# Kernel tuning notes

Hardware: AMD Instinct MI355X
Metric: run time of the kernel (lower is better)

## Reference

```python
import jax, jax.numpy as jnp
import numpy as np

NEG_SLOPE = 0.2
EPS = 1e-16


def gat_conv(x, edge_index, W, att_src, att_dst, bias, heads, out_ch, concat):
    """PyG-style GATConv (eval mode, add_self_loops=True)."""
    N = x.shape[0]
    h = (x @ W).reshape(N, heads, out_ch)              # [N,H,C]
    loop = jnp.arange(N, dtype=edge_index.dtype)
    src = jnp.concatenate([edge_index[0], loop])       # [E+N]
    dst = jnp.concatenate([edge_index[1], loop])
    a_src = jnp.sum(h * att_src, axis=-1)              # [N,H]
    a_dst = jnp.sum(h * att_dst, axis=-1)
    e = jax.nn.leaky_relu(a_src[src] + a_dst[dst], NEG_SLOPE)  # [E+N,H]
    # segment softmax over destination nodes
    m = jax.ops.segment_max(e, dst, num_segments=N)
    e = jnp.exp(e - m[dst])
    s = jax.ops.segment_sum(e, dst, num_segments=N)
    alpha = e / (s[dst] + EPS)                         # [E+N,H]
    msg = h[src] * alpha[..., None]                    # [E+N,H,C]
    out = jax.ops.segment_sum(msg, dst, num_segments=N)  # [N,H,C]
    out = out.reshape(N, heads * out_ch) if concat else out.mean(axis=1)
    return out + bias


def setup_inputs() -> dict:
    key = jax.random.key(0)
    ks = jax.random.split(key, 11)
    N, F, E = 100000, 128, 1600000
    H1, C1 = 4, 16
    H2, C2 = 1, 16
    return {
        "x": jax.random.normal(ks[0], (N, F), dtype=jnp.float32),
        "edge_index": jax.random.randint(ks[1], (2, E), 0, N, dtype=jnp.int64) if jax.config.jax_enable_x64 else jax.random.randint(ks[1], (2, E), 0, N).astype(jnp.int32),
        "W1": jax.random.normal(ks[2], (F, H1 * C1), dtype=jnp.float32) * 0.1,
        "att_src1": jax.random.normal(ks[3], (H1, C1), dtype=jnp.float32) * 0.1,
        "att_dst1": jax.random.normal(ks[4], (H1, C1), dtype=jnp.float32) * 0.1,
        "bias1": jax.random.normal(ks[5], (H1 * C1,), dtype=jnp.float32) * 0.1,
        "W2": jax.random.normal(ks[6], (H1 * C1, H2 * C2), dtype=jnp.float32) * 0.1,
        "att_src2": jax.random.normal(ks[7], (H2, C2), dtype=jnp.float32) * 0.1,
        "att_dst2": jax.random.normal(ks[8], (H2, C2), dtype=jnp.float32) * 0.1,
        "bias2": jax.random.normal(ks[9], (C2,), dtype=jnp.float32) * 0.1,
    }


def reference(x, edge_index, W1, att_src1, att_dst1, bias1, W2, att_src2, att_dst2, bias2):
    # dropout is identity in eval mode
    h = gat_conv(x, edge_index, W1, att_src1, att_dst1, bias1, heads=4, out_ch=16, concat=True)
    h = jax.nn.elu(h)
    h = gat_conv(h, edge_index, W2, att_src2, att_dst2, bias2, heads=1, out_ch=16, concat=False)
    return jax.nn.log_softmax(h, axis=1)
```

## Files before the change

### kernel.cpp

```cpp
#include <hip/hip_runtime.h>
#include <hip/hip_fp16.h>
#include <hip/hip_bf16.h>
#include <math.h>


#define LRELU(v) ((v) > 0.f ? (v) : 0.2f * (v))
#define BSH 8
#define BCAP 5120
#define CHK 2048
#define CAP1 64
#define CAP2 64

typedef __attribute__((ext_vector_type(8))) short short8;
typedef __attribute__((ext_vector_type(4))) float float4v;

static __device__ __forceinline__ short f2bf(float f) {
    __hip_bfloat16 b = __float2bfloat16(f);
    return *reinterpret_cast<short*>(&b);
}

__global__ __launch_bounds__(256) void k_scatter(const int* __restrict__ ei, int* __restrict__ cursor,
                                                 int* __restrict__ stage, int E, int NBK) {
    __shared__ int sval[CHK];
    __shared__ int gaddr[CHK];
    __shared__ int hist[512];
    __shared__ int lbase[512];
    __shared__ int cnt2[512];
    __shared__ int gdelta[512];
    __shared__ int sA[512];
    int tid = threadIdx.x;
    int e0 = blockIdx.x * CHK;
    int nedge = E - e0; if (nedge > CHK) nedge = CHK;

    for (int i = tid; i < 512; i += 256) { hist[i] = 0; cnt2[i] = 0; }
    __syncthreads();
    for (int j = tid; j < nedge; j += 256) {
        int d = ei[E + e0 + j];
        atomicAdd(&hist[d >> BSH], 1);
    }
    __syncthreads();
    sA[tid] = hist[tid]; sA[tid + 256] = hist[tid + 256];
    __syncthreads();
    for (int off = 1; off < 512; off <<= 1) {
        int r0 = sA[tid] + ((tid >= off) ? sA[tid - off] : 0);
        int r1 = sA[tid + 256] + ((tid + 256 >= off) ? sA[tid + 256 - off] : 0);
        __syncthreads();
        sA[tid] = r0; sA[tid + 256] = r1;
        __syncthreads();
    }
    for (int i = tid; i < 512; i += 256) lbase[i] = sA[i] - hist[i];
    __syncthreads();
    for (int b = tid; b < NBK; b += 256) {
        int c = hist[b];
        if (c > 0) {
            int rel = atomicAdd(&cursor[b], c);
            gdelta[b] = b * BCAP + rel - lbase[b];
        }
    }
    __syncthreads();
    for (int j = tid; j < nedge; j += 256) {
        int s = ei[e0 + j];
        int d = ei[E + e0 + j];
        int b = d >> BSH;
        int r = atomicAdd(&cnt2[b], 1);
        int slot = lbase[b] + r;
        sval[slot]  = s | ((d & ((1 << BSH) - 1)) << 17);
        gaddr[slot] = gdelta[b] + slot;
    }
    __syncthreads();
    for (int s = tid; s < nedge; s += 256) stage[gaddr[s]] = sval[s];
}

__global__ __launch_bounds__(256) void k_build(const int* __restrict__ stage,
                                               const int* __restrict__ cursor,
                                               int* __restrict__ row_start,
                                               int* __restrict__ csr,
                                               const float* __restrict__ W1,
                                               const float* __restrict__ att_src,
                                               const float* __restrict__ att_dst,
                                               float* __restrict__ Wc,
                                               int NBK, int E, int N) {
    __shared__ int cnt[256];
    __shared__ int lb[256];
    __shared__ int cur[256];
    __shared__ int sA[256];
    int b = blockIdx.x, tid = threadIdx.x;
    int nodes0 = b << BSH;
    int nnodes = N - nodes0; if (nnodes > 256) nnodes = 256;
    int partial = 0;
    for (int i = tid; i < b; i += 256) partial += cursor[i];
    sA[tid] = partial;
    __syncthreads();
    for (int off = 128; off >= 1; off >>= 1) {
        if (tid < off) sA[tid] += sA[tid + off];
        __syncthreads();
    }
    int ebase = sA[0];
    int ecnt = cursor[b];
    __syncthreads();
    if (b == 0) {
        if (tid == 0) row_start[N] = E + N;
        for (int i = tid; i < 16 * 128; i += 256) {
            int col = i >> 7, k = i & 127;
            float v = 0.f;
            if (col < 8) {
                int h = col & 3;
                const float* att = (col < 4) ? att_src : att_dst;
                #pragma unroll
                for (int c = 0; c < 16; c++) v += W1[k * 64 + h * 16 + c] * att[h * 16 + c];
            }
            Wc[i] = v;
        }
    }
    const int* sbk = stage + b * BCAP;
    cnt[tid] = (tid < nnodes) ? 1 : 0;
    __syncthreads();
    for (int e = tid; e < ecnt; e += 256) {
        int l = (sbk[e] >> 17) & 255;
        atomicAdd(&cnt[l], 1);
    }
    __syncthreads();
    int myc = cnt[tid];
    sA[tid] = myc;
    __syncthreads();
    for (int off = 1; off < 256; off <<= 1) {
        int r = sA[tid] + ((tid >= off) ? sA[tid - off] : 0);
        __syncthreads();
        sA[tid] = r;
        __syncthreads();
    }
    int gb = ebase + nodes0;
    lb[tid] = sA[tid] - myc;
    cur[tid] = 1;
    __syncthreads();
    if (tid < nnodes) {
        row_start[nodes0 + tid] = gb + lb[tid];
        csr[gb + lb[tid]] = nodes0 + tid;
    }
    __syncthreads();
    for (int e = tid; e < ecnt; e += 256) {
        int v = sbk[e];
        int l = (v >> 17) & 255;
        int src = v & 0x1FFFF;
        int r = atomicAdd(&cur[l], 1);
        csr[gb + lb[l] + r] = src;
    }
}

__global__ __launch_bounds__(256) void k_gemm1(const float* __restrict__ x,
                                               const float* __restrict__ W1,
                                               const float* __restrict__ Wc,
                                               __half* __restrict__ h1, float* __restrict__ a_src,
                                               float* __restrict__ a_dst, int N) {
    __shared__ short wt[80 * 136];
    int tid = threadIdx.x;
    for (int i = tid; i < 128 * 64; i += 256) {
        int k = i >> 6, c = i & 63;
        wt[c * 136 + k] = f2bf(W1[i]);
    }
    for (int i = tid; i < 16 * 128; i += 256) {
        int col = i >> 7, k = i & 127;
        wt[(64 + col) * 136 + k] = f2bf(Wc[i]);
    }
    __syncthreads();
    int wave = tid >> 6, lane = tid & 63;
    int m = lane & 15, q = lane >> 4;
    int nbase = blockIdx.x * 64 + wave * 16;
    int anode = nbase + m;
    bool rowok = anode < N;
    const float* xrow = x + (size_t)(rowok ? anode : 0) * 128 + q * 8;

    float4v acc[5];
    #pragma unroll
    for (int ct = 0; ct < 5; ct++)
        #pragma unroll
        for (int r = 0; r < 4; r++) acc[ct][r] = 0.f;

    #pragma unroll
    for (int kc = 0; kc < 4; kc++) {
        float4 u0 = make_float4(0.f, 0.f, 0.f, 0.f), u1 = u0;
        if (rowok) {
            u0 = *(const float4*)(xrow + kc * 32);
            u1 = *(const float4*)(xrow + kc * 32 + 4);
        }
        short8 af;
        af[0] = f2bf(u0.x); af[1] = f2bf(u0.y); af[2] = f2bf(u0.z); af[3] = f2bf(u0.w);
        af[4] = f2bf(u1.x); af[5] = f2bf(u1.y); af[6] = f2bf(u1.z); af[7] = f2bf(u1.w);
        #pragma unroll
        for (int ct = 0; ct < 5; ct++) {
            short8 bf = *(const short8*)&wt[(ct * 16 + m) * 136 + kc * 32 + q * 8];
            acc[ct] = __builtin_amdgcn_mfma_f32_16x16x32_bf16(af, bf, acc[ct], 0, 0, 0);
        }
    }
    #pragma unroll
    for (int ct = 0; ct < 4; ct++) {
        #pragma unroll
        for (int r = 0; r < 4; r++) {
            int n = nbase + q * 4 + r;
            if (n < N) h1[(size_t)n * 64 + ct * 16 + m] = __float2half(acc[ct][r]);
        }
    }
    #pragma unroll
    for (int r = 0; r < 4; r++) {
        int n = nbase + q * 4 + r;
        if (n < N) {
            float v = acc[4][r];
            if (m < 4) a_src[n * 4 + m] = v;
            else if (m < 8) a_dst[n * 4 + (m - 4)] = v;
        }
    }
}

__global__ __launch_bounds__(256) void k_agg1(const int* __restrict__ row_start,
                                              const int* __restrict__ csr_src,
                                              const float* __restrict__ a_src,
                                              const float* __restrict__ a_dst,
                                              const __half* __restrict__ h1,
                                              const float* __restrict__ bias,
                                              float* __restrict__ out1, int N) {
    __shared__ int   sidx[16][CAP1];
    __shared__ float sval[16][CAP1 * 4];
    int tid = threadIdx.x;
    int wave = tid >> 6, lane = tid & 63;
    int quad = lane >> 4, l16 = lane & 15;
    int slot = wave * 4 + quad;
    int node = blockIdx.x * 16 + slot;
    if (node >= N) return;
    int row = row_start[node];
    int deg = row_start[node + 1] - row;
    float4 ad = ((const float4*)a_dst)[node];
    float s0 = 0.f, s1 = 0.f, s2 = 0.f, s3 = 0.f;
    for (int j = l16; j < deg; j += 16) {
        int s = csr_src[row + j];
        float4 as = ((const float4*)a_src)[s];
        float e0 = __expf(LRELU(as.x + ad.x));
        float e1 = __expf(LRELU(as.y + ad.y));
        float e2 = __expf(LRELU(as.z + ad.z));
        float e3 = __expf(LRELU(as.w + ad.w));
        if (j < CAP1) {
            sidx[slot][j] = s;
            *(float4*)&sval[slot][j * 4] = make_float4(e0, e1, e2, e3);
        }
        s0 += e0; s1 += e1; s2 += e2; s3 += e3;
    }
    #pragma unroll
    for (int m = 1; m < 16; m <<= 1) {
        s0 += __shfl_xor(s0, m, 64);
        s1 += __shfl_xor(s1, m, 64);
        s2 += __shfl_xor(s2, m, 64);
        s3 += __shfl_xor(s3, m, 64);
    }
    int myh = l16 >> 2;
    float ssv = myh == 0 ? s0 : myh == 1 ? s1 : myh == 2 ? s2 : s3;
    float adm = myh == 0 ? ad.x : myh == 1 ? ad.y : myh == 2 ? ad.z : ad.w;
    float iv = 1.f / (ssv + 1e-16f);
    float A0 = 0.f, A1 = 0.f, A2 = 0.f, A3 = 0.f;
    float B0 = 0.f, B1 = 0.f, B2 = 0.f, B3 = 0.f;
    int dc = deg < CAP1 ? deg : CAP1;
    int j = 0;
    for (; j + 8 <= dc; j += 8) {
        int t[8]; float e[8]; float2 lo[8], hi[8];
        #pragma unroll
        for (int u = 0; u < 8; u++) {
            t[u] = sidx[slot][j + u];
            e[u] = sval[slot][(j + u) * 4 + myh];
        }
        #pragma unroll
        for (int u = 0; u < 8; u++) {
            union { float2 f; __half2 h[2]; } uu;
            uu.f = *(const float2*)&h1[(size_t)t[u] * 64 + l16 * 4];
            lo[u] = __half22float2(uu.h[0]);
            hi[u] = __half22float2(uu.h[1]);
        }
        #pragma unroll
        for (int u = 0; u < 8; u += 2) {
            A0 += e[u] * lo[u].x; A1 += e[u] * lo[u].y;
            A2 += e[u] * hi[u].x; A3 += e[u] * hi[u].y;
            B0 += e[u + 1] * lo[u + 1].x; B1 += e[u + 1] * lo[u + 1].y;
            B2 += e[u + 1] * hi[u + 1].x; B3 += e[u + 1] * hi[u + 1].y;
        }
    }
    for (; j < dc; j++) {
        int t = sidx[slot][j];
        float e = sval[slot][j * 4 + myh];
        union { float2 f; __half2 h[2]; } uu;
        uu.f = *(const float2*)&h1[(size_t)t * 64 + l16 * 4];
        float2 lo = __half22float2(uu.h[0]), hi = __half22float2(uu.h[1]);
        A0 += e * lo.x; A1 += e * lo.y; A2 += e * hi.x; A3 += e * hi.y;
    }
    for (; j < deg; j++) {
        int s = csr_src[row + j];
        float e = __expf(LRELU(a_src[s * 4 + myh] + adm));
        union { float2 f; __half2 h[2]; } uu;
        uu.f = *(const float2*)&h1[(size_t)s * 64 + l16 * 4];
        float2 lo = __half22float2(uu.h[0]), hi = __half22float2(uu.h[1]);
        A0 += e * lo.x; A1 += e * lo.y; A2 += e * hi.x; A3 += e * hi.y;
    }
    A0 += B0; A1 += B1; A2 += B2; A3 += B3;
    float4 bb = ((const float4*)bias)[l16];
    float o0 = A0 * iv + bb.x;
    float o1 = A1 * iv + bb.y;
    float o2 = A2 * iv + bb.z;
    float o3 = A3 * iv + bb.w;
    o0 = (o0 > 0.f) ? o0 : (__expf(o0) - 1.f);
    o1 = (o1 > 0.f) ? o1 : (__expf(o1) - 1.f);
    o2 = (o2 > 0.f) ? o2 : (__expf(o2) - 1.f);
    o3 = (o3 > 0.f) ? o3 : (__expf(o3) - 1.f);
    ((float4*)out1)[(size_t)node * 16 + l16] = make_float4(o0, o1, o2, o3);
}

__global__ __launch_bounds__(256) void k_gemm2(const float* __restrict__ out1,
                                               const float* __restrict__ W2,
                                               const float* __restrict__ att_src,
                                               const float* __restrict__ att_dst,
                                               __half* __restrict__ h2, float* __restrict__ a_src,
                                               float* __restrict__ a_dst, int N) {
    __shared__ float ws[64 * 16];
    __shared__ float xs[16 * 65];
    int tid = threadIdx.x;
    for (int i = tid; i < 64 * 16; i += 256) ws[i] = W2[i];
    int n0 = blockIdx.x * 16;
    for (int i = tid; i < 16 * 64; i += 256) {
        int r = i >> 6, c = i & 63;
        int n = n0 + r;
        xs[r * 65 + c] = (n < N) ? out1[(size_t)n * 64 + c] : 0.f;
    }
    __syncthreads();
    int nl = tid >> 4, c = tid & 15;
    int n = n0 + nl;
    float acc = 0.f;
    #pragma unroll
    for (int k = 0; k < 64; k++) acc += xs[nl * 65 + k] * ws[k * 16 + c];
    float asv = acc * att_src[c];
    float adv = acc * att_dst[c];
    #pragma unroll
    for (int m = 1; m < 16; m <<= 1) {
        asv += __shfl_xor(asv, m, 64);
        adv += __shfl_xor(adv, m, 64);
    }
    if (n < N) {
        h2[(size_t)n * 16 + c] = __float2half(acc);
        if (c == 0) { a_src[n] = asv; a_dst[n] = adv; }
    }
}

__global__ __launch_bounds__(256) void k_agg2(const int* __restrict__ row_start,
                                              const int* __restrict__ csr_src,
                                              const float* __restrict__ a_src,
                                              const float* __restrict__ a_dst,
                                              const __half* __restrict__ h2,
                                              const float* __restrict__ bias,
                                              float* __restrict__ out, int N) {
    __shared__ int   sidx[16][CAP2];
    __shared__ float sval[16][CAP2];
    int tid = threadIdx.x;
    int wave = tid >> 6, lane = tid & 63;
    int quad = lane >> 4, l16 = lane & 15;
    int slot = wave * 4 + quad;
    int node = blockIdx.x * 16 + slot;
    if (node >= N) return;
    int row = row_start[node];
    int deg = row_start[node + 1] - row;
    float ad = a_dst[node];
    float sh = 0.f;
    for (int j = l16; j < deg; j += 16) {
        int s = csr_src[row + j];
        float e = __expf(LRELU(a_src[s] + ad));
        if (j < CAP2) { sidx[slot][j] = s; sval[slot][j] = e; }
        sh += e;
    }
    #pragma unroll
    for (int m = 1; m < 16; m <<= 1) sh += __shfl_xor(sh, m, 64);
    float iv = 1.f / (sh + 1e-16f);
    int cg = l16 & 7, eg = l16 >> 3;
    float ax = 0.f, ay = 0.f, bx = 0.f, by = 0.f;
    int dc = deg < CAP2 ? deg : CAP2;
    int j = eg;
    for (; j + 6 < dc; j += 8) {
        int t0 = sidx[slot][j], t1 = sidx[slot][j + 2];
        int t2 = sidx[slot][j + 4], t3 = sidx[slot][j + 6];
        float e0 = sval[slot][j], e1 = sval[slot][j + 2];
        float e2 = sval[slot][j + 4], e3 = sval[slot][j + 6];
        float2 g0 = __half22float2(*(const __half2*)&h2[(size_t)t0 * 16 + cg * 2]);
        float2 g1 = __half22float2(*(const __half2*)&h2[(size_t)t1 * 16 + cg * 2]);
        float2 g2 = __half22float2(*(const __half2*)&h2[(size_t)t2 * 16 + cg * 2]);
        float2 g3 = __half22float2(*(const __half2*)&h2[(size_t)t3 * 16 + cg * 2]);
        ax += e0 * g0.x + e2 * g2.x; ay += e0 * g0.y + e2 * g2.y;
        bx += e1 * g1.x + e3 * g3.x; by += e1 * g1.y + e3 * g3.y;
    }
    for (; j < deg; j += 2) {
        int s; float e;
        if (j < dc) { s = sidx[slot][j]; e = sval[slot][j]; }
        else { s = csr_src[row + j]; e = __expf(LRELU(a_src[s] + ad)); }
        float2 g = __half22float2(*(const __half2*)&h2[(size_t)s * 16 + cg * 2]);
        ax += e * g.x; ay += e * g.y;
    }
    ax += bx; ay += by;
    ax += __shfl_xor(ax, 8, 64);
    ay += __shfl_xor(ay, 8, 64);
    float2 bb = ((const float2*)bias)[cg];
    float vx = ax * iv + bb.x;
    float vy = ay * iv + bb.y;
    float mx = fmaxf(vx, vy);
    #pragma unroll
    for (int m = 1; m < 8; m <<= 1) mx = fmaxf(mx, __shfl_xor(mx, m, 64));
    float se = __expf(vx - mx) + __expf(vy - mx);
    #pragma unroll
    for (int m = 1; m < 8; m <<= 1) se += __shfl_xor(se, m, 64);
    float ls = mx + __logf(se);
    if (eg == 0)
        ((float2*)out)[(size_t)node * 8 + cg] = make_float2(vx - ls, vy - ls);
}

extern "C" void kernel_launch(void* const* d_in, const int* in_sizes, int n_in,
                              void* d_out, int out_size, void* d_ws, size_t ws_size,
                              hipStream_t stream) {
    const float* x        = (const float*)d_in[0];
    const int*   ei       = (const int*)d_in[1];
    const float* W1       = (const float*)d_in[2];
    const float* att_src1 = (const float*)d_in[3];
    const float* att_dst1 = (const float*)d_in[4];
    const float* bias1    = (const float*)d_in[5];
    const float* W2       = (const float*)d_in[6];
    const float* att_src2 = (const float*)d_in[7];
    const float* att_dst2 = (const float*)d_in[8];
    const float* bias2    = (const float*)d_in[9];
    float* out = (float*)d_out;

    const int N = in_sizes[0] / 128;
    const int E = in_sizes[1] / 2;
    const int NBK = (N + 255) >> BSH;

    char* p = (char*)d_ws;
    auto alloc = [&](size_t bytes) -> void* {
        void* r = (void*)p;
        p += (bytes + 255) & ~(size_t)255;
        return r;
    };
    __half* h1     = (__half*)alloc((size_t)N * 64 * 2);
    float* out1    = (float*)alloc((size_t)N * 64 * 4);
    __half* h2     = (__half*)alloc((size_t)N * 16 * 2);
    float* a_src1  = (float*)alloc((size_t)N * 4 * 4);
    float* a_dst1  = (float*)alloc((size_t)N * 4 * 4);
    float* a_src2  = (float*)alloc((size_t)N * 4);
    float* a_dst2  = (float*)alloc((size_t)N * 4);
    float* Wc      = (float*)alloc(16 * 128 * 4);
    int*   row_st  = (int*)alloc((size_t)(N + 1) * 4);
    int*   csr     = (int*)alloc((size_t)(E + N) * 4);
    int*   stage   = (int*)alloc((size_t)NBK * BCAP * 4);
    int*   cursor  = (int*)alloc((size_t)NBK * 4);
    (void)ws_size; (void)n_in; (void)out_size;

    hipMemsetAsync(cursor, 0, (size_t)NBK * 4, stream);
    k_scatter<<<(E + CHK - 1) / CHK, 256, 0, stream>>>(ei, cursor, stage, E, NBK);
    k_build<<<NBK, 256, 0, stream>>>(stage, cursor, row_st, csr,
                                     W1, att_src1, att_dst1, Wc, NBK, E, N);
    k_gemm1<<<(N + 63) / 64, 256, 0, stream>>>(x, W1, Wc, h1, a_src1, a_dst1, N);
    k_agg1<<<(N + 15) / 16, 256, 0, stream>>>(row_st, csr, a_src1, a_dst1, h1, bias1, out1, N);
    k_gemm2<<<(N + 15) / 16, 256, 0, stream>>>(out1, W2, att_src2, att_dst2, h2, a_src2, a_dst2, N);
    k_agg2<<<(N + 15) / 16, 256, 0, stream>>>(row_st, csr, a_src2, a_dst2, h2, bias2, out, N);
}
```

Before: 256.5 us.

## Store layer-1 output in fp16, use MFMA for gemm2, simplify edge scatter

The ELU output of layer 1 is now stored as fp16, which halves the traffic between agg1 and gemm2. gemm2 is rewritten to use fp16 MFMA 16x16x32, with the attention projections folded into precomputed Wc2 columns computed in k_build. k_scatter drops its LDS prefix-sum and staging buffers and writes directly to global slots, with larger chunks (CHK 8192). The fp16 intermediate adds rounding error, and the direct scatter writes are less coalesced.

After: 237.2 us (median of 2 runs). 7.5% less time.

```diff
diff --git a/kernel.cpp b/kernel.cpp
--- a/kernel.cpp
+++ b/kernel.cpp
@@ -7,11 +7,12 @@
 #define LRELU(v) ((v) > 0.f ? (v) : 0.2f * (v))
 #define BSH 8
 #define BCAP 5120
-#define CHK 2048
+#define CHK 8192
 #define CAP1 64
 #define CAP2 64
 
 typedef __attribute__((ext_vector_type(8))) short short8;
+typedef __attribute__((ext_vector_type(8))) _Float16 half8;
 typedef __attribute__((ext_vector_type(4))) float float4v;
 
 static __device__ __forceinline__ short f2bf(float f) {
@@ -21,13 +22,9 @@
 
 __global__ __launch_bounds__(256) void k_scatter(const int* __restrict__ ei, int* __restrict__ cursor,
                                                  int* __restrict__ stage, int E, int NBK) {
-    __shared__ int sval[CHK];
-    __shared__ int gaddr[CHK];
     __shared__ int hist[512];
-    __shared__ int lbase[512];
     __shared__ int cnt2[512];
-    __shared__ int gdelta[512];
-    __shared__ int sA[512];
+    __shared__ int base[512];
     int tid = threadIdx.x;
     int e0 = blockIdx.x * CHK;
     int nedge = E - e0; if (nedge > CHK) nedge = CHK;
@@ -39,23 +36,9 @@
         atomicAdd(&hist[d >> BSH], 1);
     }
     __syncthreads();
-    sA[tid] = hist[tid]; sA[tid + 256] = hist[tid + 256];
-    __syncthreads();
-    for (int off = 1; off < 512; off <<= 1) {
-        int r0 = sA[tid] + ((tid >= off) ? sA[tid - off] : 0);
-        int r1 = sA[tid + 256] + ((tid + 256 >= off) ? sA[tid + 256 - off] : 0);
-        __syncthreads();
-        sA[tid] = r0; sA[tid + 256] = r1;
-        __syncthreads();
-    }
-    for (int i = tid; i < 512; i += 256) lbase[i] = sA[i] - hist[i];
-    __syncthreads();
     for (int b = tid; b < NBK; b += 256) {
         int c = hist[b];
-        if (c > 0) {
-            int rel = atomicAdd(&cursor[b], c);
-            gdelta[b] = b * BCAP + rel - lbase[b];
-        }
+        if (c > 0) base[b] = b * BCAP + atomicAdd(&cursor[b], c);
     }
     __syncthreads();
     for (int j = tid; j < nedge; j += 256) {
@@ -63,12 +46,8 @@
         int d = ei[E + e0 + j];
         int b = d >> BSH;
         int r = atomicAdd(&cnt2[b], 1);
-        int slot = lbase[b] + r;
-        sval[slot]  = s | ((d & ((1 << BSH) - 1)) << 17);
-        gaddr[slot] = gdelta[b] + slot;
-    }
-    __syncthreads();
-    for (int s = tid; s < nedge; s += 256) stage[gaddr[s]] = sval[s];
+        stage[base[b] + r] = s | ((d & ((1 << BSH) - 1)) << 17);
+    }
 }
 
 __global__ __launch_bounds__(256) void k_build(const int* __restrict__ stage,
@@ -79,6 +58,10 @@
                                                const float* __restrict__ att_src,
                                                const float* __restrict__ att_dst,
                                                float* __restrict__ Wc,
+                                               const float* __restrict__ W2,
+                                               const float* __restrict__ att_src2,
+                                               const float* __restrict__ att_dst2,
+                                               float* __restrict__ Wc2,
                                                int NBK, int E, int N) {
     __shared__ int cnt[256];
     __shared__ int lb[256];
@@ -111,6 +94,14 @@
             }
             Wc[i] = v;
         }
+        for (int i = tid; i < 128; i += 256) {
+            int col = i >> 6, k = i & 63;
+            const float* att = col ? att_dst2 : att_src2;
+            float v = 0.f;
+            #pragma unroll
+            for (int c = 0; c < 16; c++) v += W2[k * 16 + c] * att[c];
+            Wc2[i] = v;
+        }
     }
     const int* sbk = stage + b * BCAP;
     cnt[tid] = (tid < nnodes) ? 1 : 0;
@@ -217,7 +208,7 @@
                                               const float* __restrict__ a_dst,
                                               const __half* __restrict__ h1,
                                               const float* __restrict__ bias,
-                                              float* __restrict__ out1, int N) {
+                                              __half* __restrict__ out1, int N) {
     __shared__ int   sidx[16][CAP1];
     __shared__ float sval[16][CAP1 * 4];
     int tid = threadIdx.x;
@@ -306,41 +297,53 @@
     o1 = (o1 > 0.f) ? o1 : (__expf(o1) - 1.f);
     o2 = (o2 > 0.f) ? o2 : (__expf(o2) - 1.f);
     o3 = (o3 > 0.f) ? o3 : (__expf(o3) - 1.f);
-    ((float4*)out1)[(size_t)node * 16 + l16] = make_float4(o0, o1, o2, o3);
-}
-
-__global__ __launch_bounds__(256) void k_gemm2(const float* __restrict__ out1,
+    union { __half2 h2v[2]; float2 f2; } pk;
+    pk.h2v[0] = __floats2half2_rn(o0, o1);
+    pk.h2v[1] = __floats2half2_rn(o2, o3);
+    *(float2*)&out1[(size_t)node * 64 + l16 * 4] = pk.f2;
+}
+
+__global__ __launch_bounds__(256) void k_gemm2(const __half* __restrict__ out1,
                                                const float* __restrict__ W2,
-                                               const float* __restrict__ att_src,
-                                               const float* __restrict__ att_dst,
+                                               const float* __restrict__ Wc2,
                                                __half* __restrict__ h2, float* __restrict__ a_src,
                                                float* __restrict__ a_dst, int N) {
-    __shared__ float ws[64 * 16];
-    __shared__ float xs[16 * 65];
+    __shared__ _Float16 wt2[16][72];
+    __shared__ _Float16 wtb[16][72];
     int tid = threadIdx.x;
-    for (int i = tid; i < 64 * 16; i += 256) ws[i] = W2[i];
-    int n0 = blockIdx.x * 16;
     for (int i = tid; i < 16 * 64; i += 256) {
-        int r = i >> 6, c = i & 63;
-        int n = n0 + r;
-        xs[r * 65 + c] = (n < N) ? out1[(size_t)n * 64 + c] : 0.f;
-    }
-    __syncthreads();
-    int nl = tid >> 4, c = tid & 15;
-    int n = n0 + nl;
-    float acc = 0.f;
-    #pragma unroll
-    for (int k = 0; k < 64; k++) acc += xs[nl * 65 + k] * ws[k * 16 + c];
-    float asv = acc * att_src[c];
-    float adv = acc * att_dst[c];
-    #pragma unroll
-    for (int m = 1; m < 16; m <<= 1) {
-        asv += __shfl_xor(asv, m, 64);
-        adv += __shfl_xor(adv, m, 64);
-    }
-    if (n < N) {
-        h2[(size_t)n * 16 + c] = __float2half(acc);
-        if (c == 0) { a_src[n] = asv; a_dst[n] = adv; }
+        int k = i >> 4, c = i & 15;
+        wt2[c][k] = (_Float16)W2[i];
+    }
+    for (int i = tid; i < 16 * 64; i += 256) {
+        int col = i >> 6, k = i & 63;
+        wtb[col][k] = (col < 2) ? (_Float16)Wc2[col * 64 + k] : (_Float16)0.f;
+    }
+    __syncthreads();
+    int wave = tid >> 6, lane = tid & 63;
+    int m = lane & 15, q = lane >> 4;
+    int nbase = blockIdx.x * 64 + wave * 16;
+    int anode = nbase + m;
+    bool ok = anode < N;
+    const __half* arow = out1 + (size_t)(ok ? anode : 0) * 64 + q * 8;
+
+    float4v c1 = {0.f, 0.f, 0.f, 0.f}, c2v = {0.f, 0.f, 0.f, 0.f};
+    #pragma unroll
+    for (int kc = 0; kc < 2; kc++) {
+        half8 af = *(const half8*)(arow + kc * 32);
+        half8 b1 = *(const half8*)&wt2[m][kc * 32 + q * 8];
+        half8 b2 = *(const half8*)&wtb[m][kc * 32 + q * 8];
+        c1  = __builtin_amdgcn_mfma_f32_16x16x32_f16(af, b1, c1, 0, 0, 0);
+        c2v = __builtin_amdgcn_mfma_f32_16x16x32_f16(af, b2, c2v, 0, 0, 0);
+    }
+    #pragma unroll
+    for (int r = 0; r < 4; r++) {
+        int n = nbase + q * 4 + r;
+        if (n < N) {
+            h2[(size_t)n * 16 + m] = __float2half(c1[r]);
+            if (m == 0) a_src[n] = c2v[r];
+            else if (m == 1) a_dst[n] = c2v[r];
+        }
     }
 }
 
@@ -438,13 +441,14 @@
         return r;
     };
     __half* h1     = (__half*)alloc((size_t)N * 64 * 2);
-    float* out1    = (float*)alloc((size_t)N * 64 * 4);
+    __half* out1   = (__half*)alloc((size_t)N * 64 * 2);
     __half* h2     = (__half*)alloc((size_t)N * 16 * 2);
     float* a_src1  = (float*)alloc((size_t)N * 4 * 4);
     float* a_dst1  = (float*)alloc((size_t)N * 4 * 4);
     float* a_src2  = (float*)alloc((size_t)N * 4);
     float* a_dst2  = (float*)alloc((size_t)N * 4);
     float* Wc      = (float*)alloc(16 * 128 * 4);
+    float* Wc2     = (float*)alloc(2 * 64 * 4);
     int*   row_st  = (int*)alloc((size_t)(N + 1) * 4);
     int*   csr     = (int*)alloc((size_t)(E + N) * 4);
     int*   stage   = (int*)alloc((size_t)NBK * BCAP * 4);
@@ -454,9 +458,10 @@
     hipMemsetAsync(cursor, 0, (size_t)NBK * 4, stream);
     k_scatter<<<(E + CHK - 1) / CHK, 256, 0, stream>>>(ei, cursor, stage, E, NBK);
     k_build<<<NBK, 256, 0, stream>>>(stage, cursor, row_st, csr,
-                                     W1, att_src1, att_dst1, Wc, NBK, E, N);
+                                     W1, att_src1, att_dst1, Wc,
+                                     W2, att_src2, att_dst2, Wc2, NBK, E, N);
     k_gemm1<<<(N + 63) / 64, 256, 0, stream>>>(x, W1, Wc, h1, a_src1, a_dst1, N);
     k_agg1<<<(N + 15) / 16, 256, 0, stream>>>(row_st, csr, a_src1, a_dst1, h1, bias1, out1, N);
-    k_gemm2<<<(N + 15) / 16, 256, 0, stream>>>(out1, W2, att_src2, att_dst2, h2, a_src2, a_dst2, N);
+    k_gemm2<<<(N + 63) / 64, 256, 0, stream>>>(out1, W2, Wc2, h2, a_src2, a_dst2, N);
     k_agg2<<<(N + 15) / 16, 256, 0, stream>>>(row_st, csr, a_src2, a_dst2, h2, bias2, out, N);
 }
```
